# Optimization experiments

Hardware: AMD Instinct MI355X
Metric: run time of the kernel (lower is better)

## Reference

```python
import jax, jax.numpy as jnp
import numpy as np

B, T, D, H = 2, 2048, 1024, 16
DK = D // H


def setup_inputs() -> dict:
    key = jax.random.key(0)
    ks = jax.random.split(key, 12)
    s = 0.02
    return {
        "query": jax.random.normal(ks[0], (B, T, D), jnp.float32),
        "key": jax.random.normal(ks[1], (B, T, D), jnp.float32),
        "value": jax.random.normal(ks[2], (B, T, D), jnp.float32),
        "mask": jax.random.randint(ks[3], (B, T), 0, 2) != 0,  # True = keep
        "Wq": jax.random.normal(ks[4], (D, D), jnp.float32) * s,
        "bq": jnp.zeros((D,), jnp.float32),
        "Wk": jax.random.normal(ks[5], (D, D), jnp.float32) * s,
        "bk": jnp.zeros((D,), jnp.float32),
        "Wv": jax.random.normal(ks[6], (D, D), jnp.float32) * s,
        "bv": jnp.zeros((D,), jnp.float32),
        "Wo": jax.random.normal(ks[7], (D, D), jnp.float32) * s,
        "bo": jnp.zeros((D,), jnp.float32),
    }


def _split_heads(x):
    # [B, S, D] -> [B, H, S, DK]
    b, s, _ = x.shape
    return x.reshape(b, s, H, DK).transpose(0, 2, 1, 3)


def reference(query, key, value, mask, Wq, bq, Wk, bk, Wv, bv, Wo, bo):
    # torch Linear: y = x @ W.T + b
    q = _split_heads(query @ Wq.T + bq)   # [B,H,T,DK]
    k = _split_heads(key @ Wk.T + bk)     # [B,H,S,DK]
    v = _split_heads(value @ Wv.T + bv)   # [B,H,S,DK]
    scale = 1.0 / np.sqrt(DK).astype(np.float32)
    scores = jnp.einsum('bhtd,bhsd->bhts', q, k) * scale  # [B,H,T,S]
    # key-padding mask [B,S] -> broadcast [B,1,1,S], True = keep
    scores = jnp.where(mask[:, None, None, :], scores, -jnp.inf)
    attn = jax.nn.softmax(scores, axis=-1)
    out = jnp.einsum('bhts,bhsd->bhtd', attn, v)           # [B,H,T,DK]
    out = out.transpose(0, 2, 1, 3).reshape(query.shape[0], -1, D)
    return out @ Wo.T + bo
```

## Files before the change

### kernel.cpp

```cpp
#include <hip/hip_runtime.h>
#include <stdint.h>

#define B_SZ 2
#define T_SEQ 2048
#define DMODEL 1024
#define NHEAD 16
#define DKH 64
#define M_ROWS (B_SZ * T_SEQ)

#define LDT 72

#define INP_E  4194304u
#define W_E    1048576u

typedef __bf16 bf16x8 __attribute__((ext_vector_type(8)));
typedef float  f32x4  __attribute__((ext_vector_type(4)));

__device__ __forceinline__ unsigned short f2bf(float f) {
    unsigned u = __builtin_bit_cast(unsigned, f);
    u += 0x7fffu + ((u >> 16) & 1u);
    return (unsigned short)(u >> 16);
}
__device__ __forceinline__ uint4 cvt8(const float* p) {
    float4 f0 = *(const float4*)p, f1 = *(const float4*)(p + 4);
    uint4 r;
    r.x = (unsigned)f2bf(f0.x) | ((unsigned)f2bf(f0.y) << 16);
    r.y = (unsigned)f2bf(f0.z) | ((unsigned)f2bf(f0.w) << 16);
    r.z = (unsigned)f2bf(f1.x) | ((unsigned)f2bf(f1.y) << 16);
    r.w = (unsigned)f2bf(f1.z) | ((unsigned)f2bf(f1.w) << 16);
    return r;
}

__device__ __forceinline__ void async16(const unsigned short* g, unsigned short* l) {
    __builtin_amdgcn_global_load_lds(
        (const __attribute__((address_space(1))) void*)g,
        (__attribute__((address_space(3))) void*)l, 16, 0, 0);
}

__global__ __launch_bounds__(256) void cvt_all(
    const float* __restrict__ q, const float* __restrict__ k, const float* __restrict__ v,
    const float* __restrict__ wq, const float* __restrict__ wk,
    const float* __restrict__ wv, const float* __restrict__ wo,
    unsigned short* __restrict__ wsb)
{
    int blk = blockIdx.x;
    const float* src; unsigned short* dst; int lb;
    if      (blk < 2048) { src = q;  dst = wsb;                       lb = blk; }
    else if (blk < 4096) { src = k;  dst = wsb + INP_E;               lb = blk - 2048; }
    else if (blk < 6144) { src = v;  dst = wsb + 2 * INP_E;           lb = blk - 4096; }
    else if (blk < 6656) { src = wq; dst = wsb + 3 * INP_E;           lb = blk - 6144; }
    else if (blk < 7168) { src = wk; dst = wsb + 3 * INP_E + W_E;     lb = blk - 6656; }
    else if (blk < 7680) { src = wv; dst = wsb + 3 * INP_E + 2 * W_E; lb = blk - 7168; }
    else                 { src = wo; dst = wsb + 3 * INP_E + 3 * W_E; lb = blk - 7680; }
    size_t i = ((size_t)lb * 256 + threadIdx.x) * 8;
    *(uint4*)&dst[i] = cvt8(src + i);
}

template<int C_MODE, int MT>
__device__ __forceinline__ void gemm_core(
    const unsigned short* __restrict__ A, const unsigned short* __restrict__ W,
    const float* __restrict__ bias, void* __restrict__ C,
    int N, int K, int bx, int by,
    unsigned short* sA, unsigned short* sB)
{
    const int tid  = threadIdx.x;
    const int wave = tid >> 6, lane = tid & 63;
    const int quad = lane >> 4, l15 = lane & 15;
    const int TM = MT * 32;
    const int m0 = by * TM, n0 = bx * 128;
    const int wm = (wave & 1) * (MT * 16), wn = (wave >> 1) * 64;

    f32x4 acc[MT][4] = {};

    for (int k0 = 0; k0 < K; k0 += 64) {
        __syncthreads();
        #pragma unroll
        for (int i = 0; i < MT; i++) {
            int c   = tid + 256 * i;
            int row = c >> 3;
            int gk  = ((c & 7) ^ (row & 7)) * 8;
            int sb  = (wave * 64 + 256 * i) * 8;
            async16(&A[(size_t)(m0 + row) * K + k0 + gk], sA + sb);
        }
        #pragma unroll
        for (int i = 0; i < 4; i++) {
            int c   = tid + 256 * i;
            int row = c >> 3;
            int gk  = ((c & 7) ^ (row & 7)) * 8;
            int sb  = (wave * 64 + 256 * i) * 8;
            async16(&W[(size_t)(n0 + row) * K + k0 + gk], sB + sb);
        }
        __syncthreads();
        const int sw = l15 & 7;
        #pragma unroll
        for (int ks = 0; ks < 2; ks++) {
            bf16x8 af[MT], bfv[4];
            #pragma unroll
            for (int mt = 0; mt < MT; mt++)
                af[mt] = *(const bf16x8*)&sA[(wm + mt * 16 + l15) * 64 +
                                             (((ks * 4 + quad) ^ sw) * 8)];
            #pragma unroll
            for (int nt = 0; nt < 4; nt++)
                bfv[nt] = *(const bf16x8*)&sB[(wn + nt * 16 + l15) * 64 +
                                              (((ks * 4 + quad) ^ sw) * 8)];
            #pragma unroll
            for (int mt = 0; mt < MT; mt++)
                #pragma unroll
                for (int nt = 0; nt < 4; nt++)
                    acc[mt][nt] = __builtin_amdgcn_mfma_f32_16x16x32_bf16(
                        af[mt], bfv[nt], acc[mt][nt], 0, 0, 0);
        }
    }

    if (C_MODE == 2) {
        #pragma unroll
        for (int mt = 0; mt < MT; mt++) {
            #pragma unroll
            for (int r = 0; r < 4; r++) {
                int m = m0 + wm + mt * 16 + quad * 4 + r;
                float bm = bias[m];
                #pragma unroll
                for (int nt = 0; nt < 4; nt++) {
                    int n = n0 + wn + nt * 16 + l15;
                    int bb = n >> 11, t = n & 2047;
                    ((unsigned short*)C)[((size_t)bb * 1024 + m) * 2048 + t] =
                        f2bf(acc[mt][nt][r] + bm);
                }
            }
        }
    } else {
        #pragma unroll
        for (int nt = 0; nt < 4; nt++) {
            int n = n0 + wn + nt * 16 + l15;
            float bv = bias[n];
            #pragma unroll
            for (int mt = 0; mt < MT; mt++) {
                #pragma unroll
                for (int r = 0; r < 4; r++) {
                    int m = m0 + wm + mt * 16 + quad * 4 + r;
                    float val = acc[mt][nt][r] + bv;
                    if (C_MODE == 1) ((float*)C)[(size_t)m * N + n] = val;
                    else ((unsigned short*)C)[(size_t)m * N + n] = f2bf(val);
                }
            }
        }
    }
}

__global__ __launch_bounds__(256) void gemm_qkv(
    const unsigned short* __restrict__ Qb, const unsigned short* __restrict__ Kb,
    const unsigned short* __restrict__ Vb,
    const unsigned short* __restrict__ Wqb, const unsigned short* __restrict__ Wkb,
    const unsigned short* __restrict__ Wvb,
    const float* __restrict__ bq, const float* __restrict__ bk, const float* __restrict__ bv,
    unsigned short* __restrict__ Qp, unsigned short* __restrict__ Kp,
    unsigned short* __restrict__ Vt)
{
    __shared__ __align__(16) unsigned short sA[128 * 64];
    __shared__ __align__(16) unsigned short sB[128 * 64];
    const int z = blockIdx.z, id = blockIdx.x;
    if (z < 2) {
        gemm_core<0, 4>(z ? Kb : Qb, z ? Wkb : Wqb, z ? bk : bq, z ? Kp : Qp,
                        DMODEL, DMODEL, id & 7, id >> 3, sA, sB);
    } else {
        gemm_core<2, 4>(Wvb, Vb, bv, Vt, M_ROWS, DMODEL, id & 31, id >> 5, sA, sB);
    }
}

__global__ __launch_bounds__(256) void gemm_o(
    const unsigned short* __restrict__ AO, const unsigned short* __restrict__ Wob,
    const float* __restrict__ bo, float* __restrict__ out)
{
    __shared__ __align__(16) unsigned short sA[64 * 64];
    __shared__ __align__(16) unsigned short sB[128 * 64];
    const int id = blockIdx.x;
    gemm_core<1, 2>(AO, Wob, bo, out, DMODEL, DMODEL, id & 7, id >> 3, sA, sB);
}

#define QBLK 128
#define KVB 64
#define AW 4

__global__ __launch_bounds__(256) void attn_kernel(
    const unsigned short* __restrict__ Qp,
    const unsigned short* __restrict__ Kp,
    const unsigned short* __restrict__ Vt,
    const int* __restrict__ maskp,
    unsigned short* __restrict__ Op)
{
    __shared__ __align__(16) unsigned short sK[2][KVB * 64];
    __shared__ __align__(16) unsigned short sV[2][KVB * 64];
    __shared__ __align__(16) unsigned short sP[AW * 32 * LDT];
    __shared__ float smf[T_SEQ];

    const int tid  = threadIdx.x;
    const int wave = tid >> 6, lane = tid & 63;
    const int quad = lane >> 4, l15 = lane & 15;
    const int qblk = blockIdx.x, h = blockIdx.y, b = blockIdx.z;

    const float SCL2 = 0.125f * 1.44269504089f;
    const float MNEG = -30000.f;

    bf16x8 aq[2][2];
    #pragma unroll
    for (int mt = 0; mt < 2; mt++) {
        const int qrow = qblk * QBLK + wave * 32 + mt * 16 + l15;
        const unsigned short* qptr =
            Qp + (size_t)(b * T_SEQ + qrow) * DMODEL + h * DKH + quad * 8;
        aq[mt][0] = *(const bf16x8*)qptr;
        aq[mt][1] = *(const bf16x8*)(qptr + 32);
    }

    const unsigned short* Kb_ = Kp + (size_t)b * T_SEQ * DMODEL + h * DKH;
    const unsigned short* VtB = Vt + ((size_t)b * DMODEL + h * DKH) * T_SEQ;

    f32x4 O[2][4] = {};
    float l_r[2][4] = {};
    unsigned short* sPw = sP + wave * 32 * LDT;

    #pragma unroll
    for (int i = 0; i < 2; i++) {
        int c   = tid + 256 * i;
        int row = c >> 3;
        int gk  = ((c & 7) ^ (row & 7)) * 8;
        int sb  = (wave * 64 + 256 * i) * 8;
        async16(&Kb_[(size_t)row * DMODEL + gk], &sK[0][sb]);
        async16(&VtB[(size_t)row * T_SEQ + gk], &sV[0][sb]);
    }
    #pragma unroll
    for (int j = 0; j < 8; j++) {
        int i = tid + 256 * j;
        smf[i] = maskp[b * T_SEQ + i] ? 0.f : MNEG;
    }
    __syncthreads();

    const int sw = l15 & 7;
    for (int t = 0; t < T_SEQ / KVB; ++t) {
        const int cur = t & 1;
        const int s0 = t * KVB;
        if (t + 1 < T_SEQ / KVB) {
            #pragma unroll
            for (int i = 0; i < 2; i++) {
                int c   = tid + 256 * i;
                int row = c >> 3;
                int gk  = ((c & 7) ^ (row & 7)) * 8;
                int sb  = (wave * 64 + 256 * i) * 8;
                async16(&Kb_[(size_t)(s0 + KVB + row) * DMODEL + gk], &sK[cur ^ 1][sb]);
                async16(&VtB[(size_t)row * T_SEQ + s0 + KVB + gk], &sV[cur ^ 1][sb]);
            }
        }

        f32x4 S[2][4];
        __builtin_amdgcn_s_setprio(1);
        #pragma unroll
        for (int nt = 0; nt < 4; nt++) {
            const unsigned short* kr = &sK[cur][(nt * 16 + l15) * 64];
            const bf16x8 kf0 = *(const bf16x8*)&kr[(quad ^ sw) * 8];
            const bf16x8 kf1 = *(const bf16x8*)&kr[((quad + 4) ^ sw) * 8];
            #pragma unroll
            for (int mt = 0; mt < 2; mt++) {
                f32x4 z = {};
                z = __builtin_amdgcn_mfma_f32_16x16x32_bf16(aq[mt][0], kf0, z, 0, 0, 0);
                z = __builtin_amdgcn_mfma_f32_16x16x32_bf16(aq[mt][1], kf1, z, 0, 0, 0);
                S[mt][nt] = z;
            }
        }
        __builtin_amdgcn_s_setprio(0);

        #pragma unroll
        for (int mt = 0; mt < 2; mt++) {
            #pragma unroll
            for (int nt = 0; nt < 4; nt++) {
                float madd = smf[s0 + nt * 16 + l15];
                #pragma unroll
                for (int r = 0; r < 4; r++) {
                    float p = __builtin_amdgcn_exp2f(fmaf(S[mt][nt][r], SCL2, madd));
                    l_r[mt][r] += p;
                    unsigned u = __builtin_bit_cast(unsigned, p) + 0x8000u;
                    sPw[(mt * 16 + quad * 4 + r) * LDT + nt * 16 + l15] =
                        (unsigned short)(u >> 16);
                }
            }
        }

        bf16x8 ap0[2], ap1[2];
        #pragma unroll
        for (int mt = 0; mt < 2; mt++) {
            ap0[mt] = *(const bf16x8*)&sPw[(mt * 16 + l15) * LDT + quad * 8];
            ap1[mt] = *(const bf16x8*)&sPw[(mt * 16 + l15) * LDT + 32 + quad * 8];
        }
        __builtin_amdgcn_s_setprio(1);
        #pragma unroll
        for (int nt = 0; nt < 4; nt++) {
            const unsigned short* vr = &sV[cur][(nt * 16 + l15) * 64];
            const bf16x8 vf0 = *(const bf16x8*)&vr[(quad ^ sw) * 8];
            const bf16x8 vf1 = *(const bf16x8*)&vr[((quad + 4) ^ sw) * 8];
            #pragma unroll
            for (int mt = 0; mt < 2; mt++) {
                O[mt][nt] = __builtin_amdgcn_mfma_f32_16x16x32_bf16(
                    ap0[mt], vf0, O[mt][nt], 0, 0, 0);
                O[mt][nt] = __builtin_amdgcn_mfma_f32_16x16x32_bf16(
                    ap1[mt], vf1, O[mt][nt], 0, 0, 0);
            }
        }
        __builtin_amdgcn_s_setprio(0);

        __syncthreads();
    }

    #pragma unroll
    for (int mt = 0; mt < 2; mt++) {
        #pragma unroll
        for (int r = 0; r < 4; r++) {
            float l = l_r[mt][r];
            l += __shfl_xor(l, 1);
            l += __shfl_xor(l, 2);
            l += __shfl_xor(l, 4);
            l += __shfl_xor(l, 8);
            l_r[mt][r] = 1.0f / fmaxf(l, 1e-30f);
        }
        #pragma unroll
        for (int nt = 0; nt < 4; nt++) {
            #pragma unroll
            for (int r = 0; r < 4; r++) {
                int q = qblk * QBLK + wave * 32 + mt * 16 + quad * 4 + r;
                Op[(size_t)(b * T_SEQ + q) * DMODEL + h * DKH + nt * 16 + l15] =
                    f2bf(O[mt][nt][r] * l_r[mt][r]);
            }
        }
    }
}

template<int A_BF16, int W_BF16, int C_MODE>
__global__ __launch_bounds__(256) void gemm_bt_cvt(
    const void* __restrict__ A_, const void* __restrict__ W_,
    const float* __restrict__ bias, void* __restrict__ C_,
    int M, int N, int K)
{
    __shared__ __align__(16) unsigned short sA[128 * LDT];
    __shared__ __align__(16) unsigned short sB[128 * LDT];
    const int tid  = threadIdx.x;
    const int wave = tid >> 6, lane = tid & 63;
    const int quad = lane >> 4, l15 = lane & 15;
    const int m0 = blockIdx.y * 128, n0 = blockIdx.x * 128;
    const int wm = (wave & 1) * 64, wn = (wave >> 1) * 64;
    f32x4 acc[4][4] = {};
    for (int k0 = 0; k0 < K; k0 += 64) {
        __syncthreads();
        #pragma unroll
        for (int i = 0; i < 4; i++) {
            int c = tid + 256 * i;
            int row = c >> 3, koff = (c & 7) * 8;
            if (A_BF16)
                *(uint4*)&sA[row * LDT + koff] =
                    *(const uint4*)&((const unsigned short*)A_)[(size_t)(m0 + row) * K + k0 + koff];
            else
                *(uint4*)&sA[row * LDT + koff] =
                    cvt8((const float*)A_ + (size_t)(m0 + row) * K + k0 + koff);
            if (W_BF16)
                *(uint4*)&sB[row * LDT + koff] =
                    *(const uint4*)&((const unsigned short*)W_)[(size_t)(n0 + row) * K + k0 + koff];
            else
                *(uint4*)&sB[row * LDT + koff] =
                    cvt8((const float*)W_ + (size_t)(n0 + row) * K + k0 + koff);
        }
        __syncthreads();
        #pragma unroll
        for (int ks = 0; ks < 2; ks++) {
            bf16x8 af[4], bfr[4];
            #pragma unroll
            for (int mt = 0; mt < 4; mt++)
                af[mt] = *(const bf16x8*)&sA[(wm + mt * 16 + l15) * LDT + ks * 32 + quad * 8];
            #pragma unroll
            for (int nt = 0; nt < 4; nt++)
                bfr[nt] = *(const bf16x8*)&sB[(wn + nt * 16 + l15) * LDT + ks * 32 + quad * 8];
            #pragma unroll
            for (int mt = 0; mt < 4; mt++)
                #pragma unroll
                for (int nt = 0; nt < 4; nt++)
                    acc[mt][nt] = __builtin_amdgcn_mfma_f32_16x16x32_bf16(
                        af[mt], bfr[nt], acc[mt][nt], 0, 0, 0);
        }
    }
    if (C_MODE == 2) {
        #pragma unroll
        for (int mt = 0; mt < 4; mt++)
            #pragma unroll
            for (int r = 0; r < 4; r++) {
                int m = m0 + wm + mt * 16 + quad * 4 + r;
                float bm = bias[m];
                #pragma unroll
                for (int nt = 0; nt < 4; nt++) {
                    int n = n0 + wn + nt * 16 + l15;
                    int bb = n >> 11, t = n & 2047;
                    ((unsigned short*)C_)[((size_t)bb * 1024 + m) * 2048 + t] =
                        f2bf(acc[mt][nt][r] + bm);
                }
            }
    } else {
        #pragma unroll
        for (int nt = 0; nt < 4; nt++) {
            int n = n0 + wn + nt * 16 + l15;
            float bv = bias[n];
            #pragma unroll
            for (int mt = 0; mt < 4; mt++)
                #pragma unroll
                for (int r = 0; r < 4; r++) {
                    int m = m0 + wm + mt * 16 + quad * 4 + r;
                    float val = acc[mt][nt][r] + bv;
                    if (C_MODE == 1) ((float*)C_)[(size_t)m * N + n] = val;
                    else ((unsigned short*)C_)[(size_t)m * N + n] = f2bf(val);
                }
        }
    }
}

extern "C" void kernel_launch(void* const* d_in, const int* in_sizes, int n_in,
                              void* d_out, int out_size, void* d_ws, size_t ws_size,
                              hipStream_t stream)
{
    const float* q  = (const float*)d_in[0];
    const float* k  = (const float*)d_in[1];
    const float* v  = (const float*)d_in[2];
    const int*   mk = (const int*)d_in[3];
    const float* Wq = (const float*)d_in[4];
    const float* bq = (const float*)d_in[5];
    const float* Wk = (const float*)d_in[6];
    const float* bk = (const float*)d_in[7];
    const float* Wv = (const float*)d_in[8];
    const float* bv = (const float*)d_in[9];
    const float* Wo = (const float*)d_in[10];
    const float* bo = (const float*)d_in[11];
    float* out = (float*)d_out;

    unsigned short* wsb = (unsigned short*)d_ws;
    const dim3 gA(T_SEQ / QBLK, NHEAD, B_SZ);

    if (ws_size >= (size_t)64 * 1024 * 1024) {
        unsigned short* Qb  = wsb;
        unsigned short* Kb  = wsb + INP_E;
        unsigned short* Vb  = wsb + 2 * INP_E;
        unsigned short* Wqb = wsb + 3 * INP_E;
        unsigned short* Wkb = wsb + 3 * INP_E + W_E;
        unsigned short* Wvb = wsb + 3 * INP_E + 2 * W_E;
        unsigned short* Wob = wsb + 3 * INP_E + 3 * W_E;
        unsigned short* Qp  = wsb + 4 * INP_E;
        unsigned short* Kp  = wsb + 5 * INP_E;
        unsigned short* Vt  = wsb + 6 * INP_E;
        unsigned short* AO  = wsb + 7 * INP_E;

        cvt_all<<<8192, 256, 0, stream>>>(q, k, v, Wq, Wk, Wv, Wo, wsb);
        gemm_qkv<<<dim3(256, 1, 3), 256, 0, stream>>>(
            Qb, Kb, Vb, Wqb, Wkb, Wvb, bq, bk, bv, Qp, Kp, Vt);
        attn_kernel<<<gA, 256, 0, stream>>>(Qp, Kp, Vt, mk, AO);
        gemm_o<<<dim3(512, 1, 1), 256, 0, stream>>>(AO, Wob, bo, out);
    } else {
        unsigned short* Qp = wsb;
        unsigned short* Kp = wsb + INP_E;
        unsigned short* Vt = wsb + 2 * INP_E;
        unsigned short* AO = wsb + 3 * INP_E;
        const dim3 gN(DMODEL / 128, M_ROWS / 128);
        const dim3 gV(M_ROWS / 128, DMODEL / 128);
        gemm_bt_cvt<0, 0, 0><<<gN, 256, 0, stream>>>(q, Wq, bq, Qp, M_ROWS, DMODEL, DMODEL);
        gemm_bt_cvt<0, 0, 0><<<gN, 256, 0, stream>>>(k, Wk, bk, Kp, M_ROWS, DMODEL, DMODEL);
        gemm_bt_cvt<0, 0, 2><<<gV, 256, 0, stream>>>(Wv, v, bv, Vt, DMODEL, M_ROWS, DMODEL);
        attn_kernel<<<gA, 256, 0, stream>>>(Qp, Kp, Vt, mk, AO);
        gemm_bt_cvt<1, 0, 1><<<gN, 256, 0, stream>>>(AO, Wo, bo, out, M_ROWS, DMODEL, DMODEL);
    }
}
```

Baseline: 237.9 us.

## Split KV sequence across two wave groups in attention block with reduction

The attention block grows to 512 threads (8 waves) arranged as two groups of four waves. Each group handles alternating 64-key tiles for the same 128 queries, and the partial O and row sums are combined through shared memory at the end. This doubles the waves available per query block to hide latency. In exchange it drops the double-buffered async prefetch, so loads are no longer overlapped with compute, and it adds a final shared-memory reduction.

Result: faster. 231.9 us (-2.5%).

```diff
diff --git a/kernel.cpp b/kernel.cpp
--- a/kernel.cpp
+++ b/kernel.cpp
@@ -179,22 +179,21 @@
 
 #define QBLK 128
 #define KVB 64
-#define AW 4
-
-__global__ __launch_bounds__(256) void attn_kernel(
+
+__global__ __launch_bounds__(512, 4) void attn_kernel(
     const unsigned short* __restrict__ Qp,
     const unsigned short* __restrict__ Kp,
     const unsigned short* __restrict__ Vt,
     const int* __restrict__ maskp,
     unsigned short* __restrict__ Op)
 {
-    __shared__ __align__(16) unsigned short sK[2][KVB * 64];
-    __shared__ __align__(16) unsigned short sV[2][KVB * 64];
-    __shared__ __align__(16) unsigned short sP[AW * 32 * LDT];
+    __shared__ __align__(16) unsigned short sKV[2][2][KVB * 64];
+    __shared__ __align__(16) unsigned short sP[8 * 32 * LDT];
     __shared__ float smf[T_SEQ];
 
     const int tid  = threadIdx.x;
     const int wave = tid >> 6, lane = tid & 63;
+    const int g    = wave >> 2, wl = wave & 3;
     const int quad = lane >> 4, l15 = lane & 15;
     const int qblk = blockIdx.x, h = blockIdx.y, b = blockIdx.z;
 
@@ -204,7 +203,7 @@
     bf16x8 aq[2][2];
     #pragma unroll
     for (int mt = 0; mt < 2; mt++) {
-        const int qrow = qblk * QBLK + wave * 32 + mt * 16 + l15;
+        const int qrow = qblk * QBLK + wl * 32 + mt * 16 + l15;
         const unsigned short* qptr =
             Qp + (size_t)(b * T_SEQ + qrow) * DMODEL + h * DKH + quad * 8;
         aq[mt][0] = *(const bf16x8*)qptr;
@@ -219,42 +218,35 @@
     unsigned short* sPw = sP + wave * 32 * LDT;
 
     #pragma unroll
-    for (int i = 0; i < 2; i++) {
-        int c   = tid + 256 * i;
-        int row = c >> 3;
-        int gk  = ((c & 7) ^ (row & 7)) * 8;
-        int sb  = (wave * 64 + 256 * i) * 8;
-        async16(&Kb_[(size_t)row * DMODEL + gk], &sK[0][sb]);
-        async16(&VtB[(size_t)row * T_SEQ + gk], &sV[0][sb]);
-    }
-    #pragma unroll
-    for (int j = 0; j < 8; j++) {
-        int i = tid + 256 * j;
+    for (int j = 0; j < 4; j++) {
+        int i = tid + 512 * j;
         smf[i] = maskp[b * T_SEQ + i] ? 0.f : MNEG;
     }
-    __syncthreads();
 
     const int sw = l15 & 7;
-    for (int t = 0; t < T_SEQ / KVB; ++t) {
-        const int cur = t & 1;
-        const int s0 = t * KVB;
-        if (t + 1 < T_SEQ / KVB) {
-            #pragma unroll
-            for (int i = 0; i < 2; i++) {
-                int c   = tid + 256 * i;
-                int row = c >> 3;
-                int gk  = ((c & 7) ^ (row & 7)) * 8;
-                int sb  = (wave * 64 + 256 * i) * 8;
-                async16(&Kb_[(size_t)(s0 + KVB + row) * DMODEL + gk], &sK[cur ^ 1][sb]);
-                async16(&VtB[(size_t)row * T_SEQ + s0 + KVB + gk], &sV[cur ^ 1][sb]);
-            }
-        }
+    for (int rr = 0; rr < T_SEQ / (2 * KVB); ++rr) {
+        #pragma unroll
+        for (int i = 0; i < 2; i++) {
+            int c    = tid + 512 * i;
+            int tile = c >> 9, cc = c & 511;
+            int row  = cc >> 3;
+            int gk   = ((cc & 7) ^ (row & 7)) * 8;
+            int sb   = (wave * 64 + 512 * i) * 8;
+            int key0 = rr * 128 + tile * 64;
+            async16(&Kb_[(size_t)(key0 + row) * DMODEL + gk], &sKV[0][0][0] + sb);
+            async16(&VtB[(size_t)row * T_SEQ + key0 + gk], &sKV[1][0][0] + sb);
+        }
+        __syncthreads();
+
+        const unsigned short* sKp = &sKV[0][g][0];
+        const unsigned short* sVp = &sKV[1][g][0];
+        const int s0 = (2 * rr + g) * KVB;
 
         f32x4 S[2][4];
         __builtin_amdgcn_s_setprio(1);
         #pragma unroll
         for (int nt = 0; nt < 4; nt++) {
-            const unsigned short* kr = &sK[cur][(nt * 16 + l15) * 64];
+            const unsigned short* kr = &sKp[(nt * 16 + l15) * 64];
             const bf16x8 kf0 = *(const bf16x8*)&kr[(quad ^ sw) * 8];
             const bf16x8 kf1 = *(const bf16x8*)&kr[((quad + 4) ^ sw) * 8];
             #pragma unroll
@@ -292,7 +284,7 @@
         __builtin_amdgcn_s_setprio(1);
         #pragma unroll
         for (int nt = 0; nt < 4; nt++) {
-            const unsigned short* vr = &sV[cur][(nt * 16 + l15) * 64];
+            const unsigned short* vr = &sVp[(nt * 16 + l15) * 64];
             const bf16x8 vf0 = *(const bf16x8*)&vr[(quad ^ sw) * 8];
             const bf16x8 vf1 = *(const bf16x8*)&vr[((quad + 4) ^ sw) * 8];
             #pragma unroll
@@ -317,15 +309,40 @@
             l += __shfl_xor(l, 2);
             l += __shfl_xor(l, 4);
             l += __shfl_xor(l, 8);
-            l_r[mt][r] = 1.0f / fmaxf(l, 1e-30f);
-        }
-        #pragma unroll
-        for (int nt = 0; nt < 4; nt++) {
+            l_r[mt][r] = l;
+        }
+    }
+
+    float* OM = (float*)&sKV[0][0][0];
+    float* LM = (float*)sP;
+    if (g == 1) {
+        #pragma unroll
+        for (int mt = 0; mt < 2; mt++) {
             #pragma unroll
             for (int r = 0; r < 4; r++) {
-                int q = qblk * QBLK + wave * 32 + mt * 16 + quad * 4 + r;
-                Op[(size_t)(b * T_SEQ + q) * DMODEL + h * DKH + nt * 16 + l15] =
-                    f2bf(O[mt][nt][r] * l_r[mt][r]);
+                int row = wl * 32 + mt * 16 + quad * 4 + r;
+                if (l15 == 0) LM[row] = l_r[mt][r];
+                #pragma unroll
+                for (int nt = 0; nt < 4; nt++)
+                    OM[row * 64 + nt * 16 + l15] = O[mt][nt][r];
+            }
+        }
+    }
+    __syncthreads();
+    if (g == 0) {
+        #pragma unroll
+        for (int mt = 0; mt < 2; mt++) {
+            #pragma unroll
+            for (int r = 0; r < 4; r++) {
+                int row = wl * 32 + mt * 16 + quad * 4 + r;
+                float inv = 1.0f / fmaxf(l_r[mt][r] + LM[row], 1e-30f);
+                int q = qblk * QBLK + row;
+                #pragma unroll
+                for (int nt = 0; nt < 4; nt++) {
+                    float val = (O[mt][nt][r] + OM[row * 64 + nt * 16 + l15]) * inv;
+                    Op[(size_t)(b * T_SEQ + q) * DMODEL + h * DKH + nt * 16 + l15] =
+                        f2bf(val);
+                }
             }
         }
     }
@@ -452,7 +469,7 @@
         cvt_all<<<8192, 256, 0, stream>>>(q, k, v, Wq, Wk, Wv, Wo, wsb);
         gemm_qkv<<<dim3(256, 1, 3), 256, 0, stream>>>(
             Qb, Kb, Vb, Wqb, Wkb, Wvb, bq, bk, bv, Qp, Kp, Vt);
-        attn_kernel<<<gA, 256, 0, stream>>>(Qp, Kp, Vt, mk, AO);
+        attn_kernel<<<gA, 512, 0, stream>>>(Qp, Kp, Vt, mk, AO);
         gemm_o<<<dim3(512, 1, 1), 256, 0, stream>>>(AO, Wob, bo, out);
     } else {
         unsigned short* Qp = wsb;
@@ -464,7 +481,7 @@
         gemm_bt_cvt<0, 0, 0><<<gN, 256, 0, stream>>>(q, Wq, bq, Qp, M_ROWS, DMODEL, DMODEL);
         gemm_bt_cvt<0, 0, 0><<<gN, 256, 0, stream>>>(k, Wk, bk, Kp, M_ROWS, DMODEL, DMODEL);
         gemm_bt_cvt<0, 0, 2><<<gV, 256, 0, stream>>>(Wv, v, bv, Vt, DMODEL, M_ROWS, DMODEL);
-        attn_kernel<<<gA, 256, 0, stream>>>(Qp, Kp, Vt, mk, AO);
+        attn_kernel<<<gA, 512, 0, stream>>>(Qp, Kp, Vt, mk, AO);
         gemm_bt_cvt<1, 0, 1><<<gN, 256, 0, stream>>>(AO, Wo, bo, out, M_ROWS, DMODEL, DMODEL);
     }
 }
```
